# Optimization experiments

Hardware: AMD Instinct MI355X
Metric: run time of the kernel (lower is better)

## Reference

```python
import jax, jax.numpy as jnp
import numpy as np

B_IN, B_MID, B_OUT = 30, 16, 10   # band widths: input sphere, after S2 conv, after SO3 conv
F1, F2 = 100, 100                 # feature channels
EPS = 1e-5


def _qw(b):
    """Driscoll-Healy quadrature weights over the 2b beta samples (SOFT grid)."""
    j = np.arange(2 * b)
    k = np.arange(b)
    s = (np.sin(np.pi * (2 * j[:, None] + 1) * (2 * k[None, :] + 1) / (4 * b))
         / (2 * k[None, :] + 1)).sum(1)
    return ((2.0 / b) * np.sin(np.pi * (2 * j + 1) / (4 * b)) * s).astype(np.float32)


def _wigner_d_all(l_max, betas):
    """Wigner-d matrices d^l(beta) = exp(-i beta Jy) in the |l,m> basis (m = -l..l).
    Returns list over l of real arrays [n_beta, 2l+1, 2l+1]."""
    betas = np.asarray(betas, np.float64)
    out = []
    for l in range(l_max):
        m = np.arange(-l, l + 1)
        dim = 2 * l + 1
        Jp = np.zeros((dim, dim))
        for i in range(dim - 1):
            Jp[i + 1, i] = np.sqrt(l * (l + 1) - m[i] * (m[i] + 1))
        Jy = (Jp - Jp.T) / 2j
        ev, V = np.linalg.eigh(Jy)
        ph = np.exp(-1j * betas[:, None] * ev[None, :])
        d = np.einsum('ak,bk,ck->bac', V, ph, V.conj())
        out.append(np.real(d).astype(np.float32))
    return out


def _project(x, b):
    """Radial max-projection of a point cloud [B,3,N] onto a (beta,alpha) grid -> [B,1,2b,2b]."""
    r = jnp.sqrt(jnp.sum(x * x, axis=1) + 1e-12)                       # [B,N]
    beta = jnp.arccos(jnp.clip(x[:, 2] / r, -1 + 1e-7, 1 - 1e-7))      # [0,pi]
    alpha = jnp.mod(jnp.arctan2(x[:, 1], x[:, 0]), 2 * np.pi)          # [0,2pi)
    jb = jnp.clip((beta / np.pi * (2 * b)).astype(jnp.int32), 0, 2 * b - 1)
    ja = jnp.clip((alpha / (2 * np.pi) * (2 * b)).astype(jnp.int32), 0, 2 * b - 1)
    flat = jb * (2 * b) + ja
    img = jax.vmap(lambda f, v: jnp.zeros((2 * b) ** 2, x.dtype).at[f].max(v))(flat, r)
    return img.reshape(x.shape[0], 1, 2 * b, 2 * b)


def _s2_fft(x, dm0_w):
    """x: [B,F,2b,2b] (beta,alpha) -> list over l of x_hat [B,F,2l+1] (complex)."""
    X = jnp.fft.fft(x, axis=-1)     # FFT over alpha
    n = x.shape[-1]
    hats = []
    for l, dw in enumerate(dm0_w):
        idx = np.mod(np.arange(-l, l + 1), n)
        hats.append(jnp.einsum('pm,BFpm->BFm', jnp.asarray(dw), X[..., idx]))
    return hats


def _so3_fft(x, dmn_w):
    """x: [B,F,2b,2b,2b] (beta,alpha,gamma) -> list over l of [B,F,2l+1,2l+1]."""
    X = jnp.fft.fftn(x, axes=(-2, -1))   # FFT over alpha, gamma
    n = x.shape[-1]
    hats = []
    for l, dw in enumerate(dmn_w):
        idx = np.mod(np.arange(-l, l + 1), n)
        Xl = X[:, :, :, idx[:, None], idx[None, :]]        # [B,F,2b,2l+1,2l+1]
        hats.append(jnp.einsum('pmn,BFpmn->BFmn', jnp.asarray(dw), Xl))
    return hats


def _so3_ifft(hats, b, d_list):
    """list over l of [B,F,2l+1,2l+1] -> real SO(3) signal [B,F,2b,2b,2b]."""
    Bb, Ff = hats[0].shape[:2]
    n = 2 * b
    Fg = jnp.zeros((Bb, Ff, n, n, n), jnp.complex64)   # (beta, m, n) freq grid
    for l, h in enumerate(hats):
        idx = np.mod(np.arange(-l, l + 1), n)
        c = (2 * l + 1) * jnp.einsum('pmn,BFmn->BFpmn', jnp.asarray(d_list[l]), h)
        Fg = Fg.at[:, :, :, idx[:, None], idx[None, :]].add(c)
    return jnp.real(jnp.fft.ifft2(Fg, axes=(-2, -1)))


def _bn_relu(x, g, b):
    mu = jnp.mean(x, axis=(0, 2, 3, 4), keepdims=True)
    var = jnp.var(x, axis=(0, 2, 3, 4), keepdims=True)
    xn = (x - mu) * jax.lax.rsqrt(var + EPS)
    return jax.nn.relu(xn * g[None, :, None, None, None] + b[None, :, None, None, None])


def _forward(x, w_s2, b_s2, bn1_gamma, bn1_beta, w_so3, b_so3, bn2_gamma, bn2_beta):
    # constant tables (numpy, computed eagerly)
    betas_in = (np.arange(2 * B_IN) + 0.5) * np.pi / (2 * B_IN)
    betas_mid = (np.arange(2 * B_MID) + 0.5) * np.pi / (2 * B_MID)
    betas_out = (np.arange(2 * B_OUT) + 0.5) * np.pi / (2 * B_OUT)
    w_in, w_mid, w_out = _qw(B_IN), _qw(B_MID), _qw(B_OUT)
    d_in = _wigner_d_all(B_MID, betas_in)
    d_mid = _wigner_d_all(B_MID, betas_mid)
    d_out = _wigner_d_all(B_OUT, betas_out)
    d_eq = _wigner_d_all(B_MID, np.array([np.pi / 2]))   # equatorial grid beta = pi/2

    img = _project(x, B_IN)                              # [B,1,60,60]

    # ---- S2 convolution: band 30 -> 16 ----
    dm0_w = [d_in[l][:, :, l] * w_in[:, None] for l in range(B_MID)]   # d^l_{m0} * quad weights
    xhat = _s2_fft(img, dm0_w)                           # list of [B,1,2l+1]
    k_s2 = w_s2.shape[-1]
    a_s2 = 2 * np.pi * np.arange(k_s2) / k_s2
    ws = w_s2 * np.float32(1.0 / np.sqrt(k_s2 * 1 * B_MID ** 4 / B_IN ** 2))
    zhat = []
    for l in range(B_MID):
        m = np.arange(-l, l + 1)
        sh = (d_eq[l][0][:, l][None, :] * np.exp(-1j * np.outer(a_s2, m))).astype(np.complex64)  # [k,m]
        yh = jnp.einsum('km,iok->mio', jnp.asarray(sh), ws)           # kernel spectrum [2l+1,f_in,f_out]
        zhat.append(jnp.einsum('Bim,nio->Bomn', xhat[l], jnp.conj(yh)))  # outer product m x n
    z = _so3_ifft(zhat, B_MID, d_mid) + b_s2[None, :, None, None, None]  # [B,100,32,32,32]
    z = _bn_relu(z, bn1_gamma, bn1_beta)

    # ---- SO3 convolution: band 16 -> 10 ----
    dmn_w = [d_mid[l] * w_mid[:, None, None] for l in range(B_OUT)]
    xhat2 = _so3_fft(z, dmn_w)                           # list of [B,100,2l+1,2l+1]
    k_so3 = w_so3.shape[-1]
    a_so3 = 2 * np.pi * np.arange(k_so3) / k_so3
    wk = w_so3 * np.float32(1.0 / np.sqrt(k_so3 * F1 * B_OUT ** 3 / B_MID ** 3))
    zhat2 = []
    for l in range(B_OUT):
        m = np.arange(-l, l + 1)
        U = (d_eq[l][0][None] * np.exp(-1j * np.outer(a_so3, m))[:, :, None]).astype(np.complex64)  # [k,m,n], gamma=0
        yh = jnp.einsum('kmn,iok->mnio', jnp.asarray(U), wk)
        zhat2.append(jnp.einsum('Bimk,nkio->Bomn', xhat2[l], jnp.conj(yh)))  # z^l = x^l y^l+
    z2 = _so3_ifft(zhat2, B_OUT, d_out) + b_so3[None, :, None, None, None]   # [B,100,20,20,20]
    z2 = _bn_relu(z2, bn2_gamma, bn2_beta)

    # ---- so3_integrate: sum over alpha/gamma, quadrature-weighted sum over beta ----
    return jnp.einsum('BCpag,p->BC', z2, jnp.asarray(w_out))   # [B,100]


def setup_inputs() -> dict:
    key = jax.random.key(0)
    k0, k1, k2 = jax.random.split(key, 3)
    B, N = 8, 2048
    return {
        "x": jax.random.normal(k0, (B, 3, N), jnp.float32),
        "w_s2": jax.random.normal(k1, (1, F1, 2 * B_IN), jnp.float32),
        "b_s2": jnp.zeros((F1,), jnp.float32),
        "bn1_gamma": jnp.ones((F1,), jnp.float32),
        "bn1_beta": jnp.zeros((F1,), jnp.float32),
        "w_so3": jax.random.normal(k2, (F1, F2, 2 * B_MID), jnp.float32),
        "b_so3": jnp.zeros((F2,), jnp.float32),
        "bn2_gamma": jnp.ones((F2,), jnp.float32),
        "bn2_beta": jnp.zeros((F2,), jnp.float32),
    }


def reference(x, w_s2, b_s2, bn1_gamma, bn1_beta, w_so3, b_so3, bn2_gamma, bn2_beta):
    return _forward(x, w_s2, b_s2, bn1_gamma, bn1_beta, w_so3, b_so3, bn2_gamma, bn2_beta)
```

## Files before the change

### kernel.cpp

```cpp
#include <hip/hip_runtime.h>
#include <math.h>

#define PI_D 3.14159265358979323846

constexpr int NBATCH = 8;
constexpr int NPTS   = 2048;
constexpr int F1C    = 100;
constexpr int F2C    = 100;

__host__ __device__ constexpr int S2c(int l){ return l*(2*l-1)*(2*l+1)/3; }

constexpr int OFF_WIN   = 0;
constexpr int OFF_WMID  = OFF_WIN + 60;
constexpr int OFF_WOUTQ = OFF_WMID + 32;
constexpr int OFF_DM0W  = OFF_WOUTQ + 20;
constexpr int OFF_DMID  = OFF_DM0W + 60*256;
constexpr int OFF_DOUT  = OFF_DMID + 32*S2c(16);
constexpr int OFF_DEQ   = OFF_DOUT + 20*S2c(10);
constexpr int OFF_IMG   = OFF_DEQ + S2c(16);
constexpr int OFF_XF    = OFF_IMG + NBATCH*60*60;
constexpr int OFF_XHAT  = OFF_XF + NBATCH*60*31*2;
constexpr int OFF_WS2   = OFF_XHAT + NBATCH*256*2;
constexpr int OFF_BN1   = OFF_WS2 + 100*31*2;
constexpr int OFF_BN1AB = OFF_BN1 + 200;
constexpr int OFF_BN2   = OFF_BN1AB + 200;
constexpr int OFF_BN2AB = OFF_BN2 + 200;
constexpr int OFF_LUTA  = OFF_BN2AB + 200;
constexpr int OFF_LUTB  = OFF_LUTA + 1330;
constexpr int OFF_LUTC  = OFF_LUTB + 1330;
constexpr int OFF_WCONV = OFF_LUTC + 1330;
constexpr int OFF_XHAT2 = OFF_WCONV + 100*100*19*2;
constexpr int OFF_SBUF  = OFF_XHAT2 + NBATCH*100*S2c(10)*2;
constexpr int OFF_ZHAT2 = OFF_SBUF + NBATCH*100*S2c(10)*2;
constexpr int OFF_Z2    = OFF_ZHAT2 + NBATCH*100*S2c(10)*2;
constexpr int OFF_Z     = OFF_Z2 + NBATCH*100*20*20*20;
constexpr int WS_TOTAL  = OFF_Z + NBATCH*100*32*32*32;
constexpr int OFF_HBUF  = OFF_Z2;

__device__ __forceinline__ int S2d(int l){ return l*(2*l-1)*(2*l+1)/3; }

__global__ void k_lut(float* ws){
  int q = blockIdx.x*blockDim.x + threadIdx.x;
  if (q < 32){
    double bb = 16.0, s = 0.0;
    for (int k = 0; k < 16; ++k) s += sin(PI_D*(2*q+1)*(2*k+1)/(4.0*bb))/(2*k+1);
    ws[OFF_WMID+q] = (float)(2.0/bb * sin(PI_D*(2*q+1)/(4.0*bb)) * s);
  } else if (q < 52){
    int j = q - 32;
    double bb = 10.0, s = 0.0;
    for (int k = 0; k < 10; ++k) s += sin(PI_D*(2*j+1)*(2*k+1)/(4.0*bb))/(2*k+1);
    ws[OFF_WOUTQ+j] = (float)(2.0/bb * sin(PI_D*(2*j+1)/(4.0*bb)) * s);
  }
  if (q >= 1330) return;
  int l = 0; while (S2d(l+1) <= q) ++l;
  int loc = q - S2d(l), tl = 2*l+1;
  int mm = loc/tl, nn = loc%tl;
  ((int*)(ws+OFF_LUTA))[q] = 32*S2d(l) + mm*tl + nn;
  ((int*)(ws+OFF_LUTB))[q] = ((mm-l+9)*19 + (nn-l+9)) | ((tl*tl) << 9) | ((nn-l+9) << 19);
  ((int*)(ws+OFF_LUTC))[q] = (S2d(l) + mm*tl) | ((S2d(l) + nn*tl) << 11) | (tl << 22);
}

__device__ double dev_wigner_t(const double* fact, int l, int mp, int m, double beta){
  double ch = cos(0.5*beta), sh = sin(0.5*beta);
  int kmin = m - mp; if (kmin < 0) kmin = 0;
  int kmax = l + m; if (l - mp < kmax) kmax = l - mp;
  double pref = sqrt(fact[l+mp]*fact[l-mp]*fact[l+m]*fact[l-m]);
  int ec = 2*l + m - mp - 2*kmin, es = mp - m + 2*kmin;
  double cp = 1.0, sp = 1.0;
  for (int e = 0; e < ec; ++e) cp *= ch;
  for (int e = 0; e < es; ++e) sp *= sh;
  double ch2i = 1.0/(ch*ch), sh2 = sh*sh;
  double sum = 0.0;
  for (int k = kmin; k <= kmax; ++k){
    double t = 1.0/(fact[l+m-k]*fact[k]*fact[l-mp-k]*fact[mp-m+k]);
    if ((mp-m+k) & 1) t = -t;
    sum += t*cp*sp;
    cp *= ch2i; sp *= sh2;
  }
  return pref*sum;
}

constexpr int N_DM0W = 60*256;
constexpr int N_DMID = 32*S2c(16);
constexpr int N_DOUT = 20*S2c(10);
constexpr int N_DEQ  = S2c(16);
constexpr int N_WIG  = N_DM0W + N_DMID + N_DOUT + N_DEQ;

__global__ void k_wigner(float* ws){
  __shared__ double fact[32];
  if (threadIdx.x == 0){ fact[0] = 1.0; for (int i = 1; i < 32; ++i) fact[i] = fact[i-1]*i; }
  __syncthreads();
  int idx = blockIdx.x*blockDim.x + threadIdx.x;
  if (idx >= N_WIG) return;
  if (idx < N_DM0W){
    int l = 0; while (60*(l+1)*(l+1) <= idx) ++l;
    int rem = idx - 60*l*l, tl = 2*l+1;
    int p = rem/tl, mm = rem%tl;
    double beta = (p+0.5)*PI_D/60.0;
    double s = 0.0;
    for (int k = 0; k < 30; ++k) s += sin(PI_D*(2*p+1)*(2*k+1)/120.0)/(2*k+1);
    double w_in = (2.0/30.0) * sin(PI_D*(2*p+1)/120.0) * s;
    ws[OFF_DM0W+idx] = (float)(dev_wigner_t(fact, l, mm-l, 0, beta) * w_in);
    return;
  }
  idx -= N_DM0W;
  if (idx < N_DMID){
    int l = 0; while (32*S2d(l+1) <= idx) ++l;
    int rem = idx - 32*S2d(l), tl = 2*l+1;
    int q = rem % (tl*tl), p = rem/(tl*tl);
    int mm = q/tl, nn = q%tl;
    double beta = (p+0.5)*PI_D/32.0;
    ws[OFF_DMID+idx] = (float)dev_wigner_t(fact, l, mm-l, nn-l, beta);
    return;
  }
  idx -= N_DMID;
  if (idx < N_DOUT){
    int l = 0; while (20*S2d(l+1) <= idx) ++l;
    int rem = idx - 20*S2d(l), tl = 2*l+1;
    int q = rem % (tl*tl), p = rem/(tl*tl);
    int mm = q/tl, nn = q%tl;
    double beta = (p+0.5)*PI_D/20.0;
    ws[OFF_DOUT+idx] = (float)dev_wigner_t(fact, l, mm-l, nn-l, beta);
    return;
  }
  idx -= N_DOUT;
  {
    int l = 0; while (S2d(l+1) <= idx) ++l;
    int rem = idx - S2d(l), tl = 2*l+1;
    int mm = rem/tl, nn = rem%tl;
    ws[OFF_DEQ+idx] = (float)dev_wigner_t(fact, l, mm-l, nn-l, 0.5*PI_D);
  }
}

__global__ void k_project(const float* __restrict__ x, float* ws){
  int t = blockIdx.x*blockDim.x + threadIdx.x;
  if (t >= NBATCH*NPTS) return;
  int b = t / NPTS, n = t % NPTS;
  const float* xb = x + (size_t)b*3*NPTS;
  float xx = xb[n], yy = xb[NPTS+n], zz = xb[2*NPTS+n];
  float r = sqrtf(xx*xx + yy*yy + zz*zz + 1e-12f);
  float ct = zz / r;
  ct = fminf(fmaxf(ct, -1.0f + 1e-7f), 1.0f - 1e-7f);
  float beta = acosf(ct);
  float alpha = atan2f(yy, xx);
  if (alpha < 0.0f) alpha += 2.0f*(float)PI_D;
  int jb = (int)((beta / (float)PI_D) * 60.0f);
  jb = jb < 0 ? 0 : (jb > 59 ? 59 : jb);
  int ja = (int)((alpha / (2.0f*(float)PI_D)) * 60.0f);
  ja = ja < 0 ? 0 : (ja > 59 ? 59 : ja);
  unsigned* img = (unsigned*)(ws + OFF_IMG) + (b*3600 + jb*60 + ja);
  atomicMax(img, __float_as_uint(r));
}

__global__ void k_s2dft(float* ws){
  int t = blockIdx.x*blockDim.x + threadIdx.x;
  if (t >= NBATCH*60*31) return;
  int b = t/(60*31), r = t%(60*31);
  int p = r/31, mi = r%31, m = mi - 15;
  const float* img = ws + OFF_IMG + (b*60 + p)*60;
  float sr = 0.f, si = 0.f;
  for (int a = 0; a < 60; ++a){
    int k = ((a*m) % 60 + 60) % 60;
    float c = cospif(k/30.0f), s = sinpif(k/30.0f);
    float v = img[a];
    sr += v*c; si -= v*s;
  }
  ws[OFF_XF + t*2]   = sr;
  ws[OFF_XF + t*2+1] = si;
}

__global__ void k_xhat(float* ws){
  int t = blockIdx.x*blockDim.x + threadIdx.x;
  if (t >= NBATCH*256) return;
  int b = t/256, flat = t%256;
  int l = 0; while ((l+1)*(l+1) <= flat) ++l;
  int mm = flat - l*l, tl = 2*l+1;
  int mi = mm - l + 15;
  float sr = 0.f, si = 0.f;
  for (int p = 0; p < 60; ++p){
    float w = ws[OFF_DM0W + 60*l*l + p*tl + mm];
    sr += w * ws[OFF_XF + ((b*60+p)*31 + mi)*2];
    si += w * ws[OFF_XF + ((b*60+p)*31 + mi)*2 + 1];
  }
  ws[OFF_XHAT + t*2]   = sr;
  ws[OFF_XHAT + t*2+1] = si;
}

__global__ void k_ws2(float* ws, const float* __restrict__ w_s2, float scale1){
  int t = blockIdx.x*blockDim.x + threadIdx.x;
  if (t >= 100*31) return;
  int o = t/31, ni = t%31, n = ni - 15;
  float sr = 0.f, si = 0.f;
  for (int k = 0; k < 60; ++k){
    int kk = ((k*n) % 60 + 60) % 60;
    float c = cospif(kk/30.0f), s = sinpif(kk/30.0f);
    float v = w_s2[o*60 + k] * scale1;
    sr += v*c; si += v*s;
  }
  ws[OFF_WS2 + t*2]   = sr;
  ws[OFF_WS2 + t*2+1] = si;
}

__global__ __launch_bounds__(256) void k_H(float* ws){
  int bid = blockIdx.x;
  int p = bid & 31, b = bid >> 5;
  __shared__ float xh[512], Dt[256];
  __shared__ int dbase[16];
  int tid = threadIdx.x;
  {
    int flat = tid;
    int l = 0; while ((l+1)*(l+1) <= flat) ++l;
    int mm = flat - l*l, tl = 2*l+1;
    xh[2*flat]   = ws[OFF_XHAT + (b*256+flat)*2];
    xh[2*flat+1] = ws[OFF_XHAT + (b*256+flat)*2+1];
    Dt[flat] = (float)tl * ws[OFF_DEQ + S2d(l) + mm*tl + l];
  }
  if (tid < 16){ int l = tid, tl = 2*l+1; dbase[l] = OFF_DMID + 32*S2d(l) + p*tl*tl; }
  __syncthreads();
  float* Hb = ws + OFF_HBUF + (size_t)bid*992;
  for (int q = tid; q < 496; q += 256){
    int m = q/31, ni = q%31, n = ni-15;
    int an = n < 0 ? -n : n;
    int lmin = m > an ? m : an;
    float ar = 0.f, ai = 0.f;
    for (int l = lmin; l < 16; ++l){
      int tl = 2*l+1;
      float d = ws[dbase[l] + (m+l)*tl + (n+l)];
      float t = d * Dt[l*l + (n+l)];
      int fa = l*l + (m+l);
      ar += t*xh[2*fa]; ai += t*xh[2*fa+1];
    }
    Hb[2*q] = ar; Hb[2*q+1] = ai;
  }
}

__global__ __launch_bounds__(256) void k_so3ifft_mid(float* ws, const float* __restrict__ b_s2){
  int bid = blockIdx.x;
  int p = bid & 31, bo = bid >> 5;
  int o = bo % F1C, b = bo / F1C;
  __shared__ float Fg[992], tmpS[1024];
  __shared__ float twr[32], twi[32], Wr[31], Wi[31], redA[4], redB[4];
  int tid = threadIdx.x;
  if (tid < 32){ twr[tid] = cospif(tid/16.0f); twi[tid] = sinpif(tid/16.0f); }
  if (tid < 31){ Wr[tid] = ws[OFF_WS2 + (o*31+tid)*2]; Wi[tid] = ws[OFF_WS2 + (o*31+tid)*2+1]; }
  __syncthreads();
  {
    const float* Hb = ws + OFF_HBUF + (size_t)((b<<5)|p)*992;
    for (int q = tid; q < 496; q += 256){
      int ni = q % 31;
      float hr = Hb[2*q], hi = Hb[2*q+1];
      float wr = Wr[ni], wi = Wi[ni];
      Fg[2*q]   = hr*wr - hi*wi;
      Fg[2*q+1] = hr*wi + hi*wr;
    }
  }
  __syncthreads();
  if (tid < 128){
    int m = tid >> 3, g0 = tid & 7;
    float T0r=0,T0i=0,T1r=0,T1i=0,T2r=0,T2i=0,T3r=0,T3i=0;
    int base = 2*m*31;
    #pragma unroll
    for (int ni = 0; ni < 31; ++ni){
      int k = ((ni-15)*g0) & 31;
      float c = twr[k], s = twi[k];
      float fr = Fg[base+2*ni], fi = Fg[base+2*ni+1];
      float re = fr*c - fi*s, im = fr*s + fi*c;
      int cc = (ni+1) & 3;
      if (cc == 0){ T0r += re; T0i += im; }
      else if (cc == 1){ T1r += re; T1i += im; }
      else if (cc == 2){ T2r += re; T2i += im; }
      else { T3r += re; T3i += im; }
    }
    float Ar=T0r+T2r, Ai=T0i+T2i, Br=T0r-T2r, Bi=T0i-T2i;
    float Cr=T1r+T3r, Ci=T1i+T3i, Dr=T1r-T3r, Di=T1i-T3i;
    int ix = 2*(m*32+g0);
    tmpS[ix]      = Ar+Cr; tmpS[ix+1]    = Ai+Ci;
    tmpS[ix+16]   = Br-Di; tmpS[ix+17]   = Bi+Dr;
    tmpS[ix+32]   = Ar-Cr; tmpS[ix+33]   = Ai-Ci;
    tmpS[ix+48]   = Br+Di; tmpS[ix+49]   = Bi-Dr;
  }
  __syncthreads();
  float bsv = b_s2[o];
  float lsum = 0.f, lss = 0.f;
  float* z = ws + OFF_Z;
  size_t zb = ((size_t)(b*F1C+o)*32 + p)*1024;
  {
    int a0 = tid >> 5, g = tid & 31;
    float U0r=0, U2r=0, U1r=0, U1i=0, U3r=0, U3i=0;
    #pragma unroll
    for (int m = 1; m < 16; ++m){
      int k = (m*a0) & 31;
      float c = twr[k], s = twi[k];
      float tr = tmpS[2*(m*32+g)], ti = tmpS[2*(m*32+g)+1];
      float re = tr*c - ti*s;
      int cc = m & 3;
      if (cc == 0) U0r += re;
      else if (cc == 2) U2r += re;
      else {
        float im = tr*s + ti*c;
        if (cc == 1){ U1r += re; U1i += im; }
        else        { U3r += re; U3i += im; }
      }
    }
    float Ar = U0r + U2r, Br = U0r - U2r;
    float Cr = U1r + U3r, Di = U1i - U3i;
    float t0 = tmpS[2*g];
    float v0 = (t0 + 2.0f*(Ar + Cr))*(1.0f/1024.0f) + bsv;
    float v1 = (t0 + 2.0f*(Br - Di))*(1.0f/1024.0f) + bsv;
    float v2 = (t0 + 2.0f*(Ar - Cr))*(1.0f/1024.0f) + bsv;
    float v3 = (t0 + 2.0f*(Br + Di))*(1.0f/1024.0f) + bsv;
    z[zb + (a0     )*32 + g] = v0;
    z[zb + (a0 +  8)*32 + g] = v1;
    z[zb + (a0 + 16)*32 + g] = v2;
    z[zb + (a0 + 24)*32 + g] = v3;
    lsum = v0+v1+v2+v3;
    lss  = v0*v0+v1*v1+v2*v2+v3*v3;
  }
  for (int off = 32; off; off >>= 1){ lsum += __shfl_down(lsum, off); lss += __shfl_down(lss, off); }
  if ((tid & 63) == 0){ redA[tid>>6] = lsum; redB[tid>>6] = lss; }
  __syncthreads();
  if (tid == 0){
    atomicAdd(&ws[OFF_BN1 + o],       redA[0]+redA[1]+redA[2]+redA[3]);
    atomicAdd(&ws[OFF_BN1 + 100 + o], redB[0]+redB[1]+redB[2]+redB[3]);
  }
}

__global__ void k_bnfin1(float* ws, const float* __restrict__ g1, const float* __restrict__ be1){
  int t = threadIdx.x;
  if (t >= 100) return;
  const float invN = 1.0f/262144.0f;
  float mu = ws[OFF_BN1+t]*invN;
  float var = ws[OFF_BN1+100+t]*invN - mu*mu;
  float sA = rsqrtf(var + 1e-5f) * g1[t];
  ws[OFF_BN1AB+t]     = sA;
  ws[OFF_BN1AB+100+t] = be1[t] - mu*sA;
}

__global__ __launch_bounds__(256) void k_so3fft_a(float* ws){
  int bid = blockIdx.x;
  int p = bid & 31, bo = bid >> 5;
  int o = bo % F1C;
  __shared__ float y[32*33];
  __shared__ float Bs[32*36];
  __shared__ float t1[1216];
  __shared__ float twr[32], twi[32];
  int tid = threadIdx.x;
  if (tid < 32){ twr[tid] = cospif(tid/16.0f); twi[tid] = sinpif(tid/16.0f); }
  float sA = ws[OFF_BN1AB+o], sB = ws[OFF_BN1AB+100+o];
  float* zp = ws + OFF_Z + (size_t)bid*1024;
  {
    const float4* z4 = (const float4*)zp;
    float4 v = z4[tid];
    int a = tid >> 3, g4 = (tid & 7)*4;
    float* yr = y + a*33 + g4;
    float t0 = v.x*sA + sB, t1v = v.y*sA + sB, t2 = v.z*sA + sB, t3 = v.w*sA + sB;
    yr[0] = t0 > 0.f ? t0 : 0.f;
    yr[1] = t1v > 0.f ? t1v : 0.f;
    yr[2] = t2 > 0.f ? t2 : 0.f;
    yr[3] = t3 > 0.f ? t3 : 0.f;
  }
  __syncthreads();
  {
    int a = tid >> 3, g2 = tid & 7;
    float y0 = y[a*33+g2], y1 = y[a*33+g2+8], y2 = y[a*33+g2+16], y3 = y[a*33+g2+24];
    float e = y0+y2, f = y1+y3;
    int bb = a*36 + g2*4;
    Bs[bb]   = e+f;
    Bs[bb+1] = e-f;
    Bs[bb+2] = y0-y2;
    Bs[bb+3] = -(y1-y3);
  }
  __syncthreads();
  for (int q = tid; q < 320; q += 256){
    int a = q/10, n = q%10, ni = 9+n;
    int c = n & 3;
    int bb = a*36;
    float sr = 0.f, si = 0.f;
    if ((c & 1) == 0){
      int off = bb + (c >> 1);
      #pragma unroll
      for (int g2 = 0; g2 < 8; ++g2){
        int k = (g2*n) & 31;
        float B = Bs[off + g2*4];
        sr += B*twr[k]; si -= B*twi[k];
      }
    } else {
      float sgn = (c == 1) ? 1.f : -1.f;
      #pragma unroll
      for (int g2 = 0; g2 < 8; ++g2){
        int k = (g2*n) & 31;
        float cc_ = twr[k], ss = twi[k];
        float br = Bs[bb+g2*4+2], bi = sgn*Bs[bb+g2*4+3];
        sr += br*cc_ + bi*ss;
        si += bi*cc_ - br*ss;
      }
    }
    t1[2*(a*19+ni)] = sr; t1[2*(a*19+ni)+1] = si;
  }
  __syncthreads();
  for (int q = tid; q < 160; q += 256){
    int a = q/10, ni = 9 + q%10;
    int i0 = 2*(a*19+ni), i1 = 2*((a+16)*19+ni);
    float xr=t1[i0], xi=t1[i0+1], yr=t1[i1], yi=t1[i1+1];
    t1[i0]=xr+yr; t1[i0+1]=xi+yi; t1[i1]=xr-yr; t1[i1+1]=xi-yi;
  }
  __syncthreads();
  float wm = ws[OFF_WMID+p];
  for (int q = tid; q < 190; q += 256){
    int m = q/10 - 9, nio = q%10, ni = 9+nio;
    int off = (m & 1) ? 16*19 : 0;
    float sr = 0.f, si = 0.f;
    for (int a = 0; a < 16; ++a){
      int k = (a*m) & 31;
      float c = twr[k], s = twi[k];
      float tr = t1[2*(off+a*19+ni)], ti = t1[2*(off+a*19+ni)+1];
      sr += tr*c + ti*s;
      si += ti*c - tr*s;
    }
    sr *= wm; si *= wm;
    int qf = (m+9)*19 + ni;
    zp[2*qf] = sr; zp[2*qf+1] = si;
    if (nio > 0){
      int qm = (9-m)*19 + (9-nio);
      zp[2*qm] = sr; zp[2*qm+1] = -si;
    }
  }
}

__global__ __launch_bounds__(512) void k_so3fft_b(float* ws){
  int bo = blockIdx.x;
  int tid = threadIdx.x;
  __shared__ float xw[722];
  __shared__ float xh2[2660];
  const float* xwbase = ws + OFF_Z + (size_t)bo*32*1024;
  const int* lutA = (const int*)(ws + OFF_LUTA);
  const int* lutB = (const int*)(ws + OFF_LUTB);
  const int* lutC = (const int*)(ws + OFF_LUTC);
  float accr[3], acci[3];
  int la[3], xi2[3], tl2v[3];
  #pragma unroll
  for (int j = 0; j < 3; ++j){
    accr[j] = 0.f; acci[j] = 0.f;
    int q = tid + 512*j;
    if (q < 1330){ la[j] = lutA[q]; int lb = lutB[q]; xi2[j] = 2*(lb & 511); tl2v[j] = (lb >> 9) & 1023; }
    else { la[j] = 0; xi2[j] = 0; tl2v[j] = 0; }
  }
  for (int pp = 0; pp < 32; ++pp){
    __syncthreads();
    for (int u = tid; u < 722; u += 512) xw[u] = xwbase[pp*1024 + u];
    __syncthreads();
    #pragma unroll
    for (int j = 0; j < 3; ++j){
      int q = tid + 512*j;
      if (q < 1330){
        float d = ws[OFF_DMID + la[j] + pp*tl2v[j]];
        accr[j] += d*xw[xi2[j]]; acci[j] += d*xw[xi2[j]+1];
      }
    }
  }
  #pragma unroll
  for (int j = 0; j < 3; ++j){
    int q = tid + 512*j;
    if (q < 1330){ xh2[2*q] = accr[j]; xh2[2*q+1] = acci[j]; }
  }
  __syncthreads();
  #pragma unroll
  for (int j = 0; j < 3; ++j){
    int q = tid + 512*j;
    if (q < 1330){
      int lc = lutC[q];
      int rowstart = lc & 2047, deqrow = (lc >> 11) & 2047, tl = lc >> 22;
      const float* dq = ws + OFF_DEQ + deqrow;
      const float* xb = xh2 + 2*rowstart;
      float sr = 0.f, si = 0.f;
      for (int k = 0; k < tl; ++k){
        float d = dq[k];
        sr += d*xb[2*k]; si += d*xb[2*k+1];
      }
      int base = OFF_SBUF + (bo*1330 + q)*2;
      ws[base]   = sr;
      ws[base+1] = si;
    }
  }
}

__global__ void k_wconv(float* ws, const float* __restrict__ w_so3, float scale2){
  int t = blockIdx.x*blockDim.x + threadIdx.x;
  if (t >= 100*100*19) return;
  int ni = t % 19, io = t / 19;
  int n = ni - 9;
  float sr = 0.f, si = 0.f;
  for (int j = 0; j < 32; ++j){
    int k = (j*n) & 31;
    float c = cospif(k/16.0f), s = sinpif(k/16.0f);
    float v = w_so3[io*32 + j] * scale2;
    sr += v*c; si += v*s;
  }
  ws[OFF_WCONV + t*2]   = sr;
  ws[OFF_WCONV + t*2+1] = si;
}

__global__ void k_zhat2(float* ws){
  int t = blockIdx.x*blockDim.x + threadIdx.x;
  if (t >= NBATCH*25*1330) return;
  int q = t % 1330, boo = t / 1330;
  int oq = boo % 25, b = boo / 25;
  int o0 = oq*4;
  int lb = ((const int*)(ws+OFF_LUTB))[q];
  int ni = (lb >> 19) & 31;
  const float* sp  = ws + OFF_SBUF + (size_t)(b*100)*2660 + 2*q;
  const float* wp0 = ws + OFF_WCONV + (size_t)(o0*19 + ni)*2;
  const float* wp1 = wp0 + 38;
  const float* wp2 = wp0 + 76;
  const float* wp3 = wp0 + 114;
  float sr0=0,si0=0,sr1=0,si1=0,sr2=0,si2=0,sr3=0,si3=0;
  for (int i = 0; i < 100; ++i){
    float Sr = sp[0], Si = sp[1];
    float W0r = wp0[0], W0i = wp0[1];
    float W1r = wp1[0], W1i = wp1[1];
    float W2r = wp2[0], W2i = wp2[1];
    float W3r = wp3[0], W3i = wp3[1];
    sr0 += Sr*W0r - Si*W0i; si0 += Sr*W0i + Si*W0r;
    sr1 += Sr*W1r - Si*W1i; si1 += Sr*W1i + Si*W1r;
    sr2 += Sr*W2r - Si*W2i; si2 += Sr*W2i + Si*W2r;
    sr3 += Sr*W3r - Si*W3i; si3 += Sr*W3i + Si*W3r;
    sp += 2660;
    wp0 += 3800; wp1 += 3800; wp2 += 3800; wp3 += 3800;
  }
  size_t zb0 = (size_t)OFF_ZHAT2 + ((size_t)(b*100 + o0)*1330 + q)*2;
  ws[zb0]          = sr0; ws[zb0 + 1]      = si0;
  ws[zb0 + 2660]   = sr1; ws[zb0 + 2661]   = si1;
  ws[zb0 + 5320]   = sr2; ws[zb0 + 5321]   = si2;
  ws[zb0 + 7980]   = sr3; ws[zb0 + 7981]   = si3;
}

__global__ __launch_bounds__(256) void k_so3ifft_out(float* ws, const float* __restrict__ b_so3){
  int bid = blockIdx.x;
  int pg = bid % 4, bo = bid / 4;
  int o = bo % F2C, b = bo / F2C;
  __shared__ __align__(16) float zh[2660];
  __shared__ float Fg[380], tmpS[400];
  __shared__ float twr[20], twi[20], redA[4], redB[4];
  int tid = threadIdx.x;
  {
    const float4* zsrc = (const float4*)(ws + OFF_ZHAT2 + (size_t)bo*2660);
    float4* zds = (float4*)zh;
    for (int q = tid; q < 665; q += 256) zds[q] = zsrc[q];
  }
  if (tid < 20){ twr[tid] = cospif(tid/10.0f); twi[tid] = sinpif(tid/10.0f); }
  __syncthreads();
  float bsv = b_so3[o];
  float lsum = 0.f, lss = 0.f;
  float* z2 = ws + OFF_Z2;
  for (int pp = 0; pp < 5; ++pp){
    int p = pg*5 + pp;
    for (int q = tid; q < 190; q += 256){
      int m = q/19, ni = q%19, n = ni-9;
      int an = n < 0 ? -n : n;
      int lmin = m > an ? m : an;
      float ar = 0.f, ai = 0.f;
      for (int l = lmin; l < 10; ++l){
        int tl = 2*l+1;
        float d = ws[OFF_DOUT + 20*S2d(l) + (p*tl + (m+l))*tl + (n+l)] * (float)tl;
        int fz = S2d(l) + (m+l)*tl + (n+l);
        ar += d*zh[2*fz]; ai += d*zh[2*fz+1];
      }
      Fg[2*q] = ar; Fg[2*q+1] = ai;
    }
    __syncthreads();
    for (int q = tid; q < 100; q += 256){
      int m = q/10, g = q%10;
      float Er=0.f, Ei=0.f, Or=0.f, Oi=0.f;
      int base = 2*m*19;
      for (int ni = 1; ni < 19; ni += 2){
        int n = ni-9;
        int k = ((n*g) % 20 + 20) % 20;
        float c = twr[k], s = twi[k];
        float fr = Fg[base+2*ni], fi = Fg[base+2*ni+1];
        Er += fr*c - fi*s; Ei += fr*s + fi*c;
      }
      for (int ni = 0; ni < 19; ni += 2){
        int n = ni-9;
        int k = ((n*g) % 20 + 20) % 20;
        float c = twr[k], s = twi[k];
        float fr = Fg[base+2*ni], fi = Fg[base+2*ni+1];
        Or += fr*c - fi*s; Oi += fr*s + fi*c;
      }
      tmpS[2*(m*20+g)]      = Er+Or; tmpS[2*(m*20+g)+1]      = Ei+Oi;
      tmpS[2*(m*20+g+10)]   = Er-Or; tmpS[2*(m*20+g+10)+1]   = Ei-Oi;
    }
    __syncthreads();
    size_t zb = ((size_t)bo*20 + p)*400;
    for (int q = tid; q < 200; q += 256){
      int a = q/20, g = q%20;
      float E = 0.f, O = 0.f;
      for (int m = 2; m < 10; m += 2){
        int k = (m*a) % 20;
        E += tmpS[2*(m*20+g)]*twr[k] - tmpS[2*(m*20+g)+1]*twi[k];
      }
      for (int m = 1; m < 10; m += 2){
        int k = (m*a) % 20;
        O += tmpS[2*(m*20+g)]*twr[k] - tmpS[2*(m*20+g)+1]*twi[k];
      }
      float t0 = tmpS[2*g];
      float v1 = (t0 + 2.0f*(E+O))*(1.0f/400.0f) + bsv;
      float v2 = (t0 + 2.0f*(E-O))*(1.0f/400.0f) + bsv;
      z2[zb + a*20 + g]       = v1;
      z2[zb + (a+10)*20 + g]  = v2;
      lsum += v1+v2; lss += v1*v1+v2*v2;
    }
    __syncthreads();
  }
  for (int off = 32; off; off >>= 1){ lsum += __shfl_down(lsum, off); lss += __shfl_down(lss, off); }
  if ((tid & 63) == 0){ redA[tid>>6] = lsum; redB[tid>>6] = lss; }
  __syncthreads();
  if (tid == 0){
    atomicAdd(&ws[OFF_BN2 + o],       redA[0]+redA[1]+redA[2]+redA[3]);
    atomicAdd(&ws[OFF_BN2 + 100 + o], redB[0]+redB[1]+redB[2]+redB[3]);
  }
}

__global__ void k_bnfin2(float* ws, const float* __restrict__ g2, const float* __restrict__ be2){
  int t = threadIdx.x;
  if (t >= 100) return;
  const float invN = 1.0f/64000.0f;
  float mu = ws[OFF_BN2+t]*invN;
  float var = ws[OFF_BN2+100+t]*invN - mu*mu;
  float sA = rsqrtf(var + 1e-5f) * g2[t];
  ws[OFF_BN2AB+t]     = sA;
  ws[OFF_BN2AB+100+t] = be2[t] - mu*sA;
}

__global__ __launch_bounds__(256) void k_final(float* ws, float* __restrict__ out){
  int bid = blockIdx.x;
  int c = bid % 100, b = bid / 100;
  int tid = threadIdx.x;
  float sA = ws[OFF_BN2AB+c], sB = ws[OFF_BN2AB+100+c];
  const float4* z2 = (const float4*)(ws + OFF_Z2 + (size_t)(b*100+c)*8000);
  float lsum = 0.f;
  for (int j = tid; j < 2000; j += 256){
    int p = j / 100;
    float wq = ws[OFF_WOUTQ + p];
    float4 v = z2[j];
    float t0 = v.x*sA + sB, t1 = v.y*sA + sB, t2 = v.z*sA + sB, t3 = v.w*sA + sB;
    t0 = t0 > 0.f ? t0 : 0.f;
    t1 = t1 > 0.f ? t1 : 0.f;
    t2 = t2 > 0.f ? t2 : 0.f;
    t3 = t3 > 0.f ? t3 : 0.f;
    lsum += (t0+t1+t2+t3) * wq;
  }
  for (int off = 32; off; off >>= 1) lsum += __shfl_down(lsum, off);
  __shared__ float red[4];
  if ((tid & 63) == 0) red[tid>>6] = lsum;
  __syncthreads();
  if (tid == 0) out[b*100 + c] = red[0]+red[1]+red[2]+red[3];
}

extern "C" void kernel_launch(void* const* d_in, const int* in_sizes, int n_in,
                              void* d_out, int out_size, void* d_ws, size_t ws_size,
                              hipStream_t stream){
  const float* x      = (const float*)d_in[0];
  const float* w_s2   = (const float*)d_in[1];
  const float* b_s2   = (const float*)d_in[2];
  const float* g1     = (const float*)d_in[3];
  const float* be1    = (const float*)d_in[4];
  const float* w_so3  = (const float*)d_in[5];
  const float* b_so3  = (const float*)d_in[6];
  const float* g2     = (const float*)d_in[7];
  const float* be2    = (const float*)d_in[8];
  float* ws  = (float*)d_ws;
  float* out = (float*)d_out;

  hipMemsetAsync(ws + OFF_IMG, 0, NBATCH*3600*sizeof(float), stream);
  hipMemsetAsync(ws + OFF_BN1, 0, 200*sizeof(float), stream);
  hipMemsetAsync(ws + OFF_BN2, 0, 200*sizeof(float), stream);

  k_lut<<<6, 256, 0, stream>>>(ws);
  k_wigner<<<(N_WIG + 255)/256, 256, 0, stream>>>(ws);
  k_project<<<(NBATCH*NPTS + 255)/256, 256, 0, stream>>>(x, ws);
  k_s2dft<<<(NBATCH*60*31 + 255)/256, 256, 0, stream>>>(ws);
  k_xhat<<<(NBATCH*256 + 255)/256, 256, 0, stream>>>(ws);
  float scale1 = (float)(1.0/sqrt(60.0*1.0*65536.0/900.0));
  k_ws2<<<(100*31 + 255)/256, 256, 0, stream>>>(ws, w_s2, scale1);
  k_H<<<NBATCH*32, 256, 0, stream>>>(ws);
  k_so3ifft_mid<<<NBATCH*F1C*32, 256, 0, stream>>>(ws, b_s2);
  k_bnfin1<<<1, 128, 0, stream>>>(ws, g1, be1);
  k_so3fft_a<<<NBATCH*F1C*32, 256, 0, stream>>>(ws);
  k_so3fft_b<<<NBATCH*F1C, 512, 0, stream>>>(ws);
  float scale2 = (float)(1.0/sqrt(32.0*100.0*1000.0/4096.0));
  k_wconv<<<(100*100*19 + 255)/256, 256, 0, stream>>>(ws, w_so3, scale2);
  k_zhat2<<<(NBATCH*25*1330 + 255)/256, 256, 0, stream>>>(ws);
  k_so3ifft_out<<<NBATCH*F2C*4, 256, 0, stream>>>(ws, b_so3);
  k_bnfin2<<<1, 128, 0, stream>>>(ws, g2, be2);
  k_final<<<NBATCH*100, 256, 0, stream>>>(ws, out);
}
```

Measured before the change: 479.7 us.

## Compute BN1 statistics analytically via Parseval and fuse SO3 ifft with fft

Batch-norm statistics for the S2-conv output are now computed in the spectral domain: a small kernel sums squared magnitudes of the H coefficients per n index, then combines them with the weight norms via a Parseval-style identity. This removes the need to write the full 32^3 signal to global memory and read it back. The inverse SO3 FFT and the following BN+ReLU+forward FFT are fused into one kernel that reuses shared buffers. The risk is numerical mismatch: the Parseval identity must hold exactly for this grid, and float atomics change the summation order.

```diff
diff --git a/kernel.cpp b/kernel.cpp
--- a/kernel.cpp
+++ b/kernel.cpp
@@ -28,7 +28,8 @@
 constexpr int OFF_LUTA  = OFF_BN2AB + 200;
 constexpr int OFF_LUTB  = OFF_LUTA + 1330;
 constexpr int OFF_LUTC  = OFF_LUTB + 1330;
-constexpr int OFF_WCONV = OFF_LUTC + 1330;
+constexpr int OFF_GT    = OFF_LUTC + 1330;
+constexpr int OFF_WCONV = OFF_GT + 34;
 constexpr int OFF_XHAT2 = OFF_WCONV + 100*100*19*2;
 constexpr int OFF_SBUF  = OFF_XHAT2 + NBATCH*100*S2c(10)*2;
 constexpr int OFF_ZHAT2 = OFF_SBUF + NBATCH*100*S2c(10)*2;
@@ -234,24 +235,67 @@
   }
 }
 
-__global__ __launch_bounds__(256) void k_so3ifft_mid(float* ws, const float* __restrict__ b_s2){
+__global__ __launch_bounds__(256) void k_stats(float* ws){
+  int bid = blockIdx.x;
+  __shared__ float G[31];
+  int tid = threadIdx.x;
+  if (tid < 31) G[tid] = 0.f;
+  const float* Hb = ws + OFF_HBUF + (size_t)bid*992;
+  __syncthreads();
+  for (int q = tid; q < 496; q += 256){
+    float hr = Hb[2*q], hi = Hb[2*q+1];
+    float h2 = hr*hr + hi*hi;
+    float w = (q < 31) ? 1.f : 2.f;
+    atomicAdd(&G[q % 31], w*h2);
+  }
+  __syncthreads();
+  if (tid < 31) atomicAdd(&ws[OFF_GT + tid], G[tid]);
+  if (tid == 0){
+    atomicAdd(&ws[OFF_GT + 31], Hb[2*15]);
+    atomicAdd(&ws[OFF_GT + 32], Hb[2*15+1]);
+  }
+}
+
+__global__ void k_bnfin1(float* ws, const float* __restrict__ g1, const float* __restrict__ be1,
+                         const float* __restrict__ b_s2){
+  int t = threadIdx.x;
+  if (t >= 100) return;
+  float ssq = 0.f;
+  for (int ni = 0; ni < 31; ++ni){
+    float wr = ws[OFF_WS2 + (t*31+ni)*2], wi = ws[OFF_WS2 + (t*31+ni)*2+1];
+    ssq += (wr*wr + wi*wi) * ws[OFF_GT + ni];
+  }
+  float wr15 = ws[OFF_WS2 + (t*31+15)*2], wi15 = ws[OFF_WS2 + (t*31+15)*2+1];
+  float f00 = wr15*ws[OFF_GT+31] - wi15*ws[OFF_GT+32];
+  float bsv = b_s2[t];
+  const float invN = 1.0f/262144.0f;
+  float mu  = f00*invN + bsv;
+  float Ez2 = ssq*(invN/1024.0f) + 2.f*bsv*f00*invN + bsv*bsv;
+  float var = Ez2 - mu*mu;
+  float sA = rsqrtf(var + 1e-5f) * g1[t];
+  ws[OFF_BN1AB+t]     = sA;
+  ws[OFF_BN1AB+100+t] = be1[t] - mu*sA;
+}
+
+__global__ __launch_bounds__(256) void k_fused(float* ws, const float* __restrict__ b_s2){
   int bid = blockIdx.x;
   int p = bid & 31, bo = bid >> 5;
   int o = bo % F1C, b = bo / F1C;
-  __shared__ float Fg[992], tmpS[1024];
-  __shared__ float twr[32], twi[32], Wr[31], Wi[31], redA[4], redB[4];
+  __shared__ float A[1216], B[1152];
+  __shared__ float twr[32], twi[32], Wr[31], Wi[31];
   int tid = threadIdx.x;
   if (tid < 32){ twr[tid] = cospif(tid/16.0f); twi[tid] = sinpif(tid/16.0f); }
   if (tid < 31){ Wr[tid] = ws[OFF_WS2 + (o*31+tid)*2]; Wi[tid] = ws[OFF_WS2 + (o*31+tid)*2+1]; }
+  float sA = ws[OFF_BN1AB+o], sB = ws[OFF_BN1AB+100+o];
+  float bsv = b_s2[o];
   __syncthreads();
   {
     const float* Hb = ws + OFF_HBUF + (size_t)((b<<5)|p)*992;
     for (int q = tid; q < 496; q += 256){
       int ni = q % 31;
       float hr = Hb[2*q], hi = Hb[2*q+1];
-      float wr = Wr[ni], wi = Wi[ni];
-      Fg[2*q]   = hr*wr - hi*wi;
-      Fg[2*q+1] = hr*wi + hi*wr;
+      A[2*q]   = hr*Wr[ni] - hi*Wi[ni];
+      A[2*q+1] = hr*Wi[ni] + hi*Wr[ni];
     }
   }
   __syncthreads();
@@ -263,7 +307,7 @@
     for (int ni = 0; ni < 31; ++ni){
       int k = ((ni-15)*g0) & 31;
       float c = twr[k], s = twi[k];
-      float fr = Fg[base+2*ni], fi = Fg[base+2*ni+1];
+      float fr = A[base+2*ni], fi = A[base+2*ni+1];
       float re = fr*c - fi*s, im = fr*s + fi*c;
       int cc = (ni+1) & 3;
       if (cc == 0){ T0r += re; T0i += im; }
@@ -274,16 +318,12 @@
     float Ar=T0r+T2r, Ai=T0i+T2i, Br=T0r-T2r, Bi=T0i-T2i;
     float Cr=T1r+T3r, Ci=T1i+T3i, Dr=T1r-T3r, Di=T1i-T3i;
     int ix = 2*(m*32+g0);
-    tmpS[ix]      = Ar+Cr; tmpS[ix+1]    = Ai+Ci;
-    tmpS[ix+16]   = Br-Di; tmpS[ix+17]   = Bi+Dr;
-    tmpS[ix+32]   = Ar-Cr; tmpS[ix+33]   = Ai-Ci;
-    tmpS[ix+48]   = Br+Di; tmpS[ix+49]   = Bi-Dr;
-  }
-  __syncthreads();
-  float bsv = b_s2[o];
-  float lsum = 0.f, lss = 0.f;
-  float* z = ws + OFF_Z;
-  size_t zb = ((size_t)(b*F1C+o)*32 + p)*1024;
+    B[ix]      = Ar+Cr; B[ix+1]    = Ai+Ci;
+    B[ix+16]   = Br-Di; B[ix+17]   = Bi+Dr;
+    B[ix+32]   = Ar-Cr; B[ix+33]   = Ai-Ci;
+    B[ix+48]   = Br+Di; B[ix+49]   = Bi-Dr;
+  }
+  __syncthreads();
   {
     int a0 = tid >> 5, g = tid & 31;
     float U0r=0, U2r=0, U1r=0, U1i=0, U3r=0, U3i=0;
@@ -291,7 +331,7 @@
     for (int m = 1; m < 16; ++m){
       int k = (m*a0) & 31;
       float c = twr[k], s = twi[k];
-      float tr = tmpS[2*(m*32+g)], ti = tmpS[2*(m*32+g)+1];
+      float tr = B[2*(m*32+g)], ti = B[2*(m*32+g)+1];
       float re = tr*c - ti*s;
       int cc = m & 3;
       if (cc == 0) U0r += re;
@@ -304,71 +344,26 @@
     }
     float Ar = U0r + U2r, Br = U0r - U2r;
     float Cr = U1r + U3r, Di = U1i - U3i;
-    float t0 = tmpS[2*g];
-    float v0 = (t0 + 2.0f*(Ar + Cr))*(1.0f/1024.0f) + bsv;
-    float v1 = (t0 + 2.0f*(Br - Di))*(1.0f/1024.0f) + bsv;
-    float v2 = (t0 + 2.0f*(Ar - Cr))*(1.0f/1024.0f) + bsv;
-    float v3 = (t0 + 2.0f*(Br + Di))*(1.0f/1024.0f) + bsv;
-    z[zb + (a0     )*32 + g] = v0;
-    z[zb + (a0 +  8)*32 + g] = v1;
-    z[zb + (a0 + 16)*32 + g] = v2;
-    z[zb + (a0 + 24)*32 + g] = v3;
-    lsum = v0+v1+v2+v3;
-    lss  = v0*v0+v1*v1+v2*v2+v3*v3;
-  }
-  for (int off = 32; off; off >>= 1){ lsum += __shfl_down(lsum, off); lss += __shfl_down(lss, off); }
-  if ((tid & 63) == 0){ redA[tid>>6] = lsum; redB[tid>>6] = lss; }
-  __syncthreads();
-  if (tid == 0){
-    atomicAdd(&ws[OFF_BN1 + o],       redA[0]+redA[1]+redA[2]+redA[3]);
-    atomicAdd(&ws[OFF_BN1 + 100 + o], redB[0]+redB[1]+redB[2]+redB[3]);
-  }
-}
-
-__global__ void k_bnfin1(float* ws, const float* __restrict__ g1, const float* __restrict__ be1){
-  int t = threadIdx.x;
-  if (t >= 100) return;
-  const float invN = 1.0f/262144.0f;
-  float mu = ws[OFF_BN1+t]*invN;
-  float var = ws[OFF_BN1+100+t]*invN - mu*mu;
-  float sA = rsqrtf(var + 1e-5f) * g1[t];
-  ws[OFF_BN1AB+t]     = sA;
-  ws[OFF_BN1AB+100+t] = be1[t] - mu*sA;
-}
-
-__global__ __launch_bounds__(256) void k_so3fft_a(float* ws){
-  int bid = blockIdx.x;
-  int p = bid & 31, bo = bid >> 5;
-  int o = bo % F1C;
-  __shared__ float y[32*33];
-  __shared__ float Bs[32*36];
-  __shared__ float t1[1216];
-  __shared__ float twr[32], twi[32];
-  int tid = threadIdx.x;
-  if (tid < 32){ twr[tid] = cospif(tid/16.0f); twi[tid] = sinpif(tid/16.0f); }
-  float sA = ws[OFF_BN1AB+o], sB = ws[OFF_BN1AB+100+o];
-  float* zp = ws + OFF_Z + (size_t)bid*1024;
-  {
-    const float4* z4 = (const float4*)zp;
-    float4 v = z4[tid];
-    int a = tid >> 3, g4 = (tid & 7)*4;
-    float* yr = y + a*33 + g4;
-    float t0 = v.x*sA + sB, t1v = v.y*sA + sB, t2 = v.z*sA + sB, t3 = v.w*sA + sB;
-    yr[0] = t0 > 0.f ? t0 : 0.f;
-    yr[1] = t1v > 0.f ? t1v : 0.f;
-    yr[2] = t2 > 0.f ? t2 : 0.f;
-    yr[3] = t3 > 0.f ? t3 : 0.f;
+    float t0 = B[2*g];
+    float v0 = ((t0 + 2.0f*(Ar + Cr))*(1.0f/1024.0f) + bsv)*sA + sB;
+    float v1 = ((t0 + 2.0f*(Br - Di))*(1.0f/1024.0f) + bsv)*sA + sB;
+    float v2 = ((t0 + 2.0f*(Ar - Cr))*(1.0f/1024.0f) + bsv)*sA + sB;
+    float v3 = ((t0 + 2.0f*(Br + Di))*(1.0f/1024.0f) + bsv)*sA + sB;
+    A[(a0     )*33 + g] = v0 > 0.f ? v0 : 0.f;
+    A[(a0 +  8)*33 + g] = v1 > 0.f ? v1 : 0.f;
+    A[(a0 + 16)*33 + g] = v2 > 0.f ? v2 : 0.f;
+    A[(a0 + 24)*33 + g] = v3 > 0.f ? v3 : 0.f;
   }
   __syncthreads();
   {
     int a = tid >> 3, g2 = tid & 7;
-    float y0 = y[a*33+g2], y1 = y[a*33+g2+8], y2 = y[a*33+g2+16], y3 = y[a*33+g2+24];
+    float y0 = A[a*33+g2], y1 = A[a*33+g2+8], y2 = A[a*33+g2+16], y3 = A[a*33+g2+24];
     float e = y0+y2, f = y1+y3;
     int bb = a*36 + g2*4;
-    Bs[bb]   = e+f;
-    Bs[bb+1] = e-f;
-    Bs[bb+2] = y0-y2;
-    Bs[bb+3] = -(y1-y3);
+    B[bb]   = e+f;
+    B[bb+1] = e-f;
+    B[bb+2] = y0-y2;
+    B[bb+3] = -(y1-y3);
   }
   __syncthreads();
   for (int q = tid; q < 320; q += 256){
@@ -381,8 +376,8 @@
       #pragma unroll
       for (int g2 = 0; g2 < 8; ++g2){
         int k = (g2*n) & 31;
-        float B = Bs[off + g2*4];
-        sr += B*twr[k]; si -= B*twi[k];
+        float Bv = B[off + g2*4];
+        sr += Bv*twr[k]; si -= Bv*twi[k];
       }
     } else {
       float sgn = (c == 1) ? 1.f : -1.f;
@@ -390,22 +385,23 @@
       for (int g2 = 0; g2 < 8; ++g2){
         int k = (g2*n) & 31;
         float cc_ = twr[k], ss = twi[k];
-        float br = Bs[bb+g2*4+2], bi = sgn*Bs[bb+g2*4+3];
+        float br = B[bb+g2*4+2], bi = sgn*B[bb+g2*4+3];
         sr += br*cc_ + bi*ss;
         si += bi*cc_ - br*ss;
       }
     }
-    t1[2*(a*19+ni)] = sr; t1[2*(a*19+ni)+1] = si;
+    A[2*(a*19+ni)] = sr; A[2*(a*19+ni)+1] = si;
   }
   __syncthreads();
   for (int q = tid; q < 160; q += 256){
     int a = q/10, ni = 9 + q%10;
     int i0 = 2*(a*19+ni), i1 = 2*((a+16)*19+ni);
-    float xr=t1[i0], xi=t1[i0+1], yr=t1[i1], yi=t1[i1+1];
-    t1[i0]=xr+yr; t1[i0+1]=xi+yi; t1[i1]=xr-yr; t1[i1+1]=xi-yi;
+    float xr=A[i0], xi=A[i0+1], yr=A[i1], yi=A[i1+1];
+    A[i0]=xr+yr; A[i0+1]=xi+yi; A[i1]=xr-yr; A[i1+1]=xi-yi;
   }
   __syncthreads();
   float wm = ws[OFF_WMID+p];
+  float* zp = ws + OFF_Z + (size_t)bid*1024;
   for (int q = tid; q < 190; q += 256){
     int m = q/10 - 9, nio = q%10, ni = 9+nio;
     int off = (m & 1) ? 16*19 : 0;
@@ -413,7 +409,7 @@
     for (int a = 0; a < 16; ++a){
       int k = (a*m) & 31;
       float c = twr[k], s = twi[k];
-      float tr = t1[2*(off+a*19+ni)], ti = t1[2*(off+a*19+ni)+1];
+      float tr = A[2*(off+a*19+ni)], ti = A[2*(off+a*19+ni)+1];
       sr += tr*c + ti*s;
       si += ti*c - tr*s;
     }
@@ -672,8 +668,8 @@
   float* out = (float*)d_out;
 
   hipMemsetAsync(ws + OFF_IMG, 0, NBATCH*3600*sizeof(float), stream);
-  hipMemsetAsync(ws + OFF_BN1, 0, 200*sizeof(float), stream);
   hipMemsetAsync(ws + OFF_BN2, 0, 200*sizeof(float), stream);
+  hipMemsetAsync(ws + OFF_GT,  0, 34*sizeof(float), stream);
 
   k_lut<<<6, 256, 0, stream>>>(ws);
   k_wigner<<<(N_WIG + 255)/256, 256, 0, stream>>>(ws);
@@ -683,9 +679,9 @@
   float scale1 = (float)(1.0/sqrt(60.0*1.0*65536.0/900.0));
   k_ws2<<<(100*31 + 255)/256, 256, 0, stream>>>(ws, w_s2, scale1);
   k_H<<<NBATCH*32, 256, 0, stream>>>(ws);
-  k_so3ifft_mid<<<NBATCH*F1C*32, 256, 0, stream>>>(ws, b_s2);
-  k_bnfin1<<<1, 128, 0, stream>>>(ws, g1, be1);
-  k_so3fft_a<<<NBATCH*F1C*32, 256, 0, stream>>>(ws);
+  k_stats<<<NBATCH*32, 256, 0, stream>>>(ws);
+  k_bnfin1<<<1, 128, 0, stream>>>(ws, g1, be1, b_s2);
+  k_fused<<<NBATCH*F1C*32, 256, 0, stream>>>(ws, b_s2);
   k_so3fft_b<<<NBATCH*F1C, 512, 0, stream>>>(ws);
   float scale2 = (float)(1.0/sqrt(32.0*100.0*1000.0/4096.0));
   k_wconv<<<(100*100*19 + 255)/256, 256, 0, stream>>>(ws, w_so3, scale2);
```

Measured after the change: 448.4 us. 1.07x faster.
